# Kernel optimization log

Measured on AMD Instinct MI355X. Metric: run time of the kernel, lower is better.

## Reference

```python
import jax, jax.numpy as jnp
import numpy as np

PRECISION_WEIGHT = 3.0
FALSE_POSITIVE_PENALTY = 5.0
BATCH = 8388608
NUM_CLASSES = 2

def setup_inputs() -> dict:
    key = jax.random.key(0)
    k1, k2 = jax.random.split(key)
    logits = jax.random.normal(k1, (BATCH, NUM_CLASSES), dtype=jnp.float32)
    targets = jax.random.randint(k2, (BATCH,), 0, NUM_CLASSES, dtype=jnp.int64 if jax.config.jax_enable_x64 else jnp.int32)
    return {"logits": logits, "targets": targets}

def reference(logits, targets):
    # per-sample cross entropy: -log_softmax(logits)[target]
    logp = jax.nn.log_softmax(logits, axis=1)                     # (B, C)
    ce_loss = -jnp.take_along_axis(logp, targets[:, None].astype(jnp.int32), axis=1)[:, 0]  # (B,)
    preds = jnp.argmax(logits, axis=1)                            # (B,)
    t = targets.astype(jnp.int32)
    p = preds.astype(jnp.int32)
    # false negative (t==1, p==0) -> 1.0 ; false positive (t==0, p==1) -> 5.0 ; else 0.1
    penalty = jnp.where((t == 1) & (p == 0), 1.0,
              jnp.where((t == 0) & (p == 1), FALSE_POSITIVE_PENALTY, 0.1)).astype(logits.dtype)
    weighted = ce_loss * (1.0 + PRECISION_WEIGHT * penalty)
    return jnp.mean(weighted)
```

## Files before the change

kernel.cpp:

```cpp
#include <hip/hip_runtime.h>
#include <math.h>


#define LOSS_BATCH 8388608
#define LOSS_GRID  2048
#define LOSS_BLOCK 256

__device__ __forceinline__ float sample_loss(float l0, float l1, int t) {
    float m   = fmaxf(l0, l1);
    float d   = fabsf(l0 - l1);
    float lse = m + log1pf(__expf(-d));
    float ce  = lse - (t ? l1 : l0);
    bool p1 = l1 > l0;
    float w;
    if (t == 1 && !p1)      w = 4.0f;
    else if (t == 0 && p1)  w = 16.0f;
    else                    w = 1.3f;
    return ce * w;
}

__global__ __launch_bounds__(LOSS_BLOCK) void loss_partial_kernel(
        const float4* __restrict__ logits4,
        const int4*   __restrict__ tgt4,
        float*        __restrict__ partials)
{
    const int nquads = LOSS_BATCH / 4;
    float acc = 0.0f;
    for (int q = blockIdx.x * blockDim.x + threadIdx.x; q < nquads;
         q += gridDim.x * blockDim.x) {
        float4 a = logits4[2 * q];
        float4 b = logits4[2 * q + 1];
        int4   t = tgt4[q];
        acc += sample_loss(a.x, a.y, t.x);
        acc += sample_loss(a.z, a.w, t.y);
        acc += sample_loss(b.x, b.y, t.z);
        acc += sample_loss(b.z, b.w, t.w);
    }
    #pragma unroll
    for (int off = 32; off > 0; off >>= 1)
        acc += __shfl_down(acc, off, 64);
    __shared__ float smem[LOSS_BLOCK / 64];
    int lane = threadIdx.x & 63;
    int wid  = threadIdx.x >> 6;
    if (lane == 0) smem[wid] = acc;
    __syncthreads();
    if (threadIdx.x == 0) {
        float s = 0.0f;
        #pragma unroll
        for (int i = 0; i < LOSS_BLOCK / 64; ++i) s += smem[i];
        partials[blockIdx.x] = s;
    }
}

__global__ __launch_bounds__(256) void loss_final_kernel(
        const float* __restrict__ partials, float* __restrict__ out)
{
    double acc = 0.0;
    for (int i = threadIdx.x; i < LOSS_GRID; i += blockDim.x)
        acc += (double)partials[i];
    #pragma unroll
    for (int off = 32; off > 0; off >>= 1)
        acc += __shfl_down(acc, off, 64);
    __shared__ double smem[4];
    int lane = threadIdx.x & 63;
    int wid  = threadIdx.x >> 6;
    if (lane == 0) smem[wid] = acc;
    __syncthreads();
    if (threadIdx.x == 0) {
        double s = smem[0] + smem[1] + smem[2] + smem[3];
        out[0] = (float)(s / (double)LOSS_BATCH);
    }
}

extern "C" void kernel_launch(void* const* d_in, const int* in_sizes, int n_in,
                              void* d_out, int out_size, void* d_ws, size_t ws_size,
                              hipStream_t stream) {
    const float4* logits4 = (const float4*)d_in[0];
    const int4*   tgt4    = (const int4*)d_in[1];
    float* partials = (float*)d_ws;
    float* out      = (float*)d_out;

    loss_partial_kernel<<<LOSS_GRID, LOSS_BLOCK, 0, stream>>>(logits4, tgt4, partials);
    loss_final_kernel<<<1, 256, 0, stream>>>(partials, out);
}
```

Before: 120.3 us.

## Fuse final reduction via atomics and batch loads per thread

```diff
diff --git a/kernel.cpp b/kernel.cpp
--- a/kernel.cpp
+++ b/kernel.cpp
@@ -5,70 +5,68 @@
 #define LOSS_BATCH 8388608
 #define LOSS_GRID  2048
 #define LOSS_BLOCK 256
+#define LOSS_THREADS (LOSS_GRID * LOSS_BLOCK)
+#define QUADS_PER_THREAD 4
 
 __device__ __forceinline__ float sample_loss(float l0, float l1, int t) {
-    float m   = fmaxf(l0, l1);
-    float d   = fabsf(l0 - l1);
-    float lse = m + log1pf(__expf(-d));
-    float ce  = lse - (t ? l1 : l0);
+    float m  = fmaxf(l0, l1);
+    float d  = fabsf(l0 - l1);
+    float sp = __logf(1.0f + __expf(-d));
+    float ce = (m + sp) - (t ? l1 : l0);
     bool p1 = l1 > l0;
-    float w;
-    if (t == 1 && !p1)      w = 4.0f;
-    else if (t == 0 && p1)  w = 16.0f;
-    else                    w = 1.3f;
+    float w = 1.3f;
+    if (t) { if (!p1) w = 4.0f;  }
+    else   { if (p1)  w = 16.0f; }
     return ce * w;
 }
 
-__global__ __launch_bounds__(LOSS_BLOCK) void loss_partial_kernel(
+__global__ __launch_bounds__(LOSS_BLOCK) void loss_fused_kernel(
         const float4* __restrict__ logits4,
         const int4*   __restrict__ tgt4,
-        float*        __restrict__ partials)
+        double*       __restrict__ accum,
+        unsigned int* __restrict__ count,
+        float*        __restrict__ out)
 {
-    const int nquads = LOSS_BATCH / 4;
+    const int tid = blockIdx.x * LOSS_BLOCK + threadIdx.x;
+
+    float4 a[QUADS_PER_THREAD], b[QUADS_PER_THREAD];
+    int4   t[QUADS_PER_THREAD];
+    #pragma unroll
+    for (int k = 0; k < QUADS_PER_THREAD; ++k) {
+        const int q = tid + k * LOSS_THREADS;
+        a[k] = logits4[2 * q];
+        b[k] = logits4[2 * q + 1];
+        t[k] = tgt4[q];
+    }
+
     float acc = 0.0f;
-    for (int q = blockIdx.x * blockDim.x + threadIdx.x; q < nquads;
-         q += gridDim.x * blockDim.x) {
-        float4 a = logits4[2 * q];
-        float4 b = logits4[2 * q + 1];
-        int4   t = tgt4[q];
-        acc += sample_loss(a.x, a.y, t.x);
-        acc += sample_loss(a.z, a.w, t.y);
-        acc += sample_loss(b.x, b.y, t.z);
-        acc += sample_loss(b.z, b.w, t.w);
+    #pragma unroll
+    for (int k = 0; k < QUADS_PER_THREAD; ++k) {
+        acc += sample_loss(a[k].x, a[k].y, t[k].x);
+        acc += sample_loss(a[k].z, a[k].w, t[k].y);
+        acc += sample_loss(b[k].x, b[k].y, t[k].z);
+        acc += sample_loss(b[k].z, b[k].w, t[k].w);
     }
+
     #pragma unroll
     for (int off = 32; off > 0; off >>= 1)
         acc += __shfl_down(acc, off, 64);
     __shared__ float smem[LOSS_BLOCK / 64];
-    int lane = threadIdx.x & 63;
-    int wid  = threadIdx.x >> 6;
+    const int lane = threadIdx.x & 63;
+    const int wid  = threadIdx.x >> 6;
     if (lane == 0) smem[wid] = acc;
     __syncthreads();
+
     if (threadIdx.x == 0) {
-        float s = 0.0f;
-        #pragma unroll
-        for (int i = 0; i < LOSS_BLOCK / 64; ++i) s += smem[i];
-        partials[blockIdx.x] = s;
-    }
-}
-
-__global__ __launch_bounds__(256) void loss_final_kernel(
-        const float* __restrict__ partials, float* __restrict__ out)
-{
-    double acc = 0.0;
-    for (int i = threadIdx.x; i < LOSS_GRID; i += blockDim.x)
-        acc += (double)partials[i];
-    #pragma unroll
-    for (int off = 32; off > 0; off >>= 1)
-        acc += __shfl_down(acc, off, 64);
-    __shared__ double smem[4];
-    int lane = threadIdx.x & 63;
-    int wid  = threadIdx.x >> 6;
-    if (lane == 0) smem[wid] = acc;
-    __syncthreads();
-    if (threadIdx.x == 0) {
-        double s = smem[0] + smem[1] + smem[2] + smem[3];
-        out[0] = (float)(s / (double)LOSS_BATCH);
+        const float s = smem[0] + smem[1] + smem[2] + smem[3];
+        atomicAdd(accum, (double)s);
+        __threadfence();
+        const unsigned int pos = atomicAdd(count, 1u);
+        if (pos == LOSS_GRID - 1) {
+            __threadfence();
+            const double total = atomicAdd(accum, 0.0);
+            out[0] = (float)(total / (double)LOSS_BATCH);
+        }
     }
 }
 
@@ -77,9 +75,11 @@
                               hipStream_t stream) {
     const float4* logits4 = (const float4*)d_in[0];
     const int4*   tgt4    = (const int4*)d_in[1];
-    float* partials = (float*)d_ws;
-    float* out      = (float*)d_out;
+    double*       accum   = (double*)d_ws;
+    unsigned int* count   = (unsigned int*)((char*)d_ws + 8);
+    float*        out     = (float*)d_out;
 
-    loss_partial_kernel<<<LOSS_GRID, LOSS_BLOCK, 0, stream>>>(logits4, tgt4, partials);
-    loss_final_kernel<<<1, 256, 0, stream>>>(partials, out);
+    hipMemsetAsync(d_ws, 0, 16, stream);
+    loss_fused_kernel<<<LOSS_GRID, LOSS_BLOCK, 0, stream>>>(
+        logits4, tgt4, accum, count, out);
 }
```

Result: slower. 208.0 us (+73.0%).
